# Performance work log

Measured on AMD Instinct MI355X. Metric: run time of the kernel, lower is better.

The kernel has to match this reference:

```python
import jax, jax.numpy as jnp
import numpy as np
from jax import lax

H = 1024
E = 8
TOP_K = 2


def setup_inputs() -> dict:
    key = jax.random.key(0)
    kx, k1, k2 = jax.random.split(key, 3)
    x = jax.random.normal(kx, (8, 2048, H), dtype=jnp.float32)
    # router MLP params, init normal(0, 0.02), zero bias (matches _init_weights)
    w1 = jax.random.normal(k1, (H, 2 * H), dtype=jnp.float32) * 0.02
    b1 = jnp.zeros((2 * H,), dtype=jnp.float32)
    w2 = jax.random.normal(k2, (2 * H, E), dtype=jnp.float32) * 0.02
    b2 = jnp.zeros((E,), dtype=jnp.float32)
    return {"x": x, "w1": w1, "b1": b1, "w2": w2, "b2": b2}


def reference(x, w1, b1, w2, b2):
    # gating MLP: Linear -> GELU (exact, torch default) -> Linear
    h = jax.nn.gelu(jnp.einsum('bsh,hf->bsf', x, w1) + b1, approximate=False)
    expert_weights = jnp.einsum('bsf,fe->bse', h, w2) + b2  # [B,S,E]

    top_k_weights, top_k_indices = lax.top_k(expert_weights, TOP_K)  # [B,S,K]
    top_k_weights = jax.nn.softmax(top_k_weights, axis=-1)

    # scatter renormalized weights into dense [B,S,E] mask (indices distinct -> one-hot sum)
    onehot = jax.nn.one_hot(top_k_indices, E, dtype=expert_weights.dtype)  # [B,S,K,E]
    masks = jnp.einsum('bsk,bske->bse', top_k_weights, onehot)

    expert_usage = masks.sum(axis=(0, 1))
    expert_usage = expert_usage / expert_usage.sum()
    target_usage = jnp.full_like(expert_usage, 1.0 / E)
    load_balancing_loss = jnp.mean((expert_usage - target_usage) ** 2)

    sparsity_loss = jnp.mean(jnp.sum(masks > 0, axis=-1).astype(jnp.float32)) / TOP_K
    total_loss = load_balancing_loss + 0.1 * sparsity_loss

    return expert_weights, masks, total_loss, expert_usage
```

## Files before the change

### kernel.cpp

```cpp
#include <hip/hip_runtime.h>
#include <math.h>

#define HDIM 1024
#define FDIM 2048
#define NEXP 8
#define MTOK 16384
#define NSLC 32
#define LDSB 24576
#define LDS_BYTES (3 * 49152)

typedef __attribute__((ext_vector_type(8))) short bf16x8;
typedef __attribute__((ext_vector_type(4))) float f32x4;

__device__ inline unsigned short f2bf_rne(float f) {
    unsigned int u = __float_as_uint(f);
    u = (u + 0x7FFFu + ((u >> 16) & 1u)) >> 16;
    return (unsigned short)u;
}
__device__ inline float bf2f(unsigned short h) {
    unsigned int u = ((unsigned int)h) << 16;
    return __uint_as_float(u);
}

__global__ __launch_bounds__(256) void cvt_x(const float* __restrict__ x,
                                             unsigned short* __restrict__ af)
{
    __shared__ unsigned short hs[16384];
    __shared__ unsigned short ls[16384];
    const int mt = blockIdx.x;
    const float* src = x + (size_t)mt * 16384;
    const int m = threadIdx.x & 15;
    const int kseg = threadIdx.x >> 4;

    #pragma unroll
    for (int c = 0; c < 8; c++) {
        int k = c * 128 + kseg * 8;
        float v[8];
        *(float4*)(v)     = *(const float4*)(src + m * 1024 + k);
        *(float4*)(v + 4) = *(const float4*)(src + m * 1024 + k + 4);
        union { unsigned short u[8]; uint4 q; } oh, ol;
        #pragma unroll
        for (int j = 0; j < 8; j++) {
            unsigned short h = f2bf_rne(v[j]);
            oh.u[j] = h;
            ol.u[j] = f2bf_rne(v[j] - bf2f(h));
        }
        int kb = k >> 5, q = (k >> 3) & 3;
        int o = kb * 512 + m * 32 + q * 8;
        *(uint4*)(hs + o) = oh.q;
        *(uint4*)(ls + o) = ol.q;
    }
    __syncthreads();
    unsigned short* dst = af + (size_t)mt * 32768;
    #pragma unroll
    for (int c = 0; c < 16; c++) {
        int f = c * 2048 + threadIdx.x * 8;
        int kb = f >> 10, half = (f >> 9) & 1, idx = f & 511;
        int q = idx >> 7, mm = (idx >> 3) & 15;
        const unsigned short* s = (half ? ls : hs) + kb * 512 + mm * 32 + q * 8;
        *(uint4*)(dst + f) = *(const uint4*)s;
    }
}

__global__ __launch_bounds__(256) void cvt_w1f(const float* __restrict__ w1,
                                               unsigned short* __restrict__ wf)
{
    __shared__ float t[32][33];
    int n0 = blockIdx.x * 32;
    int k0 = blockIdx.y * 32;
    int lx = threadIdx.x & 31, ly = threadIdx.x >> 5;
    #pragma unroll
    for (int r = 0; r < 32; r += 8)
        t[ly + r][lx] = w1[(size_t)(k0 + ly + r) * FDIM + n0 + lx];
    __syncthreads();
    #pragma unroll
    for (int r = 0; r < 32; r += 8) {
        float v = t[lx][ly + r];
        unsigned short h = f2bf_rne(v);
        unsigned short l = f2bf_rne(v - bf2f(h));
        int n = n0 + ly + r, k = k0 + lx;
        size_t base = (size_t)((n >> 4) * 32 + (k >> 5)) * 1024;
        int lj = (((k >> 3) & 3) * 16 + (n & 15)) * 8 + (k & 7);
        wf[base + lj] = h;
        wf[base + 512 + lj] = l;
    }
}

#define GLDX4(gp, lofs) __builtin_amdgcn_global_load_lds( \
    (const __attribute__((address_space(1))) unsigned int*)(uintptr_t)(gp), \
    (__attribute__((address_space(3))) unsigned int*)(unsigned int)(uintptr_t)(smem + (lofs)), \
    16, 0, 0)

__global__ __launch_bounds__(512, 2) void gemm1_mfma(
    const unsigned short* __restrict__ af, const unsigned short* __restrict__ wf,
    const float* __restrict__ b1, const float* __restrict__ w2,
    float* __restrict__ part)
{
    extern __shared__ unsigned short smem[];
    const int tid  = threadIdx.x;
    const int lane = tid & 63;
    const int l15  = lane & 15;
    const int q    = lane >> 4;
    const int wave = tid >> 6;
    const int wm   = wave >> 1;
    const int wn   = wave & 1;

    const int id  = blockIdx.x;
    const int xcd = id & 7, seq = id >> 3;
    const int bn  = seq & 15;
    const int bm  = xcd * 8 + (seq >> 4);
    const int m0  = bm * 256, n0g = bn * 128;

    const unsigned short* gb[6];
    int lo[6];
    #pragma unroll
    for (int s = 0; s < 6; s++) {
        int c = wave * 6 + s;
        int f = c >> 1, half = c & 1;
        const unsigned short* base = (f < 16)
            ? af + (size_t)(bm * 16 + f) * 32768
            : wf + (size_t)(bn * 8 + (f - 16)) * 32768;
        gb[s] = base + half * 512 + lane * 8;
        lo[s] = f * 1024 + half * 512;
    }

    f32x4 acc[4][4];
    #pragma unroll
    for (int i = 0; i < 4; i++)
        #pragma unroll
        for (int j = 0; j < 4; j++) acc[i][j] = (f32x4){0.f, 0.f, 0.f, 0.f};

    #pragma unroll
    for (int s = 0; s < 6; s++) GLDX4(gb[s], lo[s]);
    #pragma unroll
    for (int s = 0; s < 6; s++) GLDX4(gb[s] + 1024, LDSB + lo[s]);
    asm volatile("s_waitcnt vmcnt(6)\n\ts_barrier" ::: "memory");

    int bo = 0;
    #pragma unroll 1
    for (int t = 0; t < 32; t++) {
        int bi = bo + 2 * LDSB; if (bi >= 3 * LDSB) bi -= 3 * LDSB;
        if (t + 2 < 32) {
            #pragma unroll
            for (int s = 0; s < 6; s++)
                GLDX4(gb[s] + (size_t)(t + 2) * 1024, bi + lo[s]);
        }
        const unsigned short* sb = smem + bo;
        bf16x8 Bh[4], Bl[4];
        #pragma unroll
        for (int j = 0; j < 4; j++) {
            Bh[j] = *(const bf16x8*)(sb + (16 + wn * 4 + j) * 1024 + lane * 8);
            Bl[j] = *(const bf16x8*)(sb + (16 + wn * 4 + j) * 1024 + 512 + lane * 8);
        }
        __builtin_amdgcn_s_setprio(1);
        #pragma unroll
        for (int ih = 0; ih < 2; ih++) {
            bf16x8 Ah[2], Al[2];
            #pragma unroll
            for (int i = 0; i < 2; i++) {
                int mt = wm * 4 + ih * 2 + i;
                Ah[i] = *(const bf16x8*)(sb + mt * 1024 + lane * 8);
                Al[i] = *(const bf16x8*)(sb + mt * 1024 + 512 + lane * 8);
            }
            #pragma unroll
            for (int i = 0; i < 2; i++)
                #pragma unroll
                for (int j = 0; j < 4; j++) {
                    f32x4 a = acc[ih * 2 + i][j];
                    a = __builtin_amdgcn_mfma_f32_16x16x32_bf16(Ah[i], Bh[j], a, 0, 0, 0);
                    a = __builtin_amdgcn_mfma_f32_16x16x32_bf16(Ah[i], Bl[j], a, 0, 0, 0);
                    a = __builtin_amdgcn_mfma_f32_16x16x32_bf16(Al[i], Bh[j], a, 0, 0, 0);
                    acc[ih * 2 + i][j] = a;
                }
        }
        __builtin_amdgcn_s_setprio(0);
        bo += LDSB; if (bo >= 3 * LDSB) bo -= 3 * LDSB;
        if (t < 30)       asm volatile("s_waitcnt vmcnt(6)\n\ts_barrier" ::: "memory");
        else if (t == 30) asm volatile("s_waitcnt vmcnt(0)\n\ts_barrier" ::: "memory");
    }

    #pragma unroll
    for (int j = 0; j < 4; j++) {
        int n = n0g + wn * 64 + j * 16 + l15;
        float bb = b1[n];
        #pragma unroll
        for (int i = 0; i < 4; i++)
            #pragma unroll
            for (int r = 0; r < 4; r++) {
                float v = acc[i][j][r] + bb;
                acc[i][j][r] = 0.5f * v * (1.0f + erff(v * 0.70710678118654752f));
            }
    }

    float w2r[4][8];
    #pragma unroll
    for (int j = 0; j < 4; j++) {
        const float4* p = (const float4*)(w2 + (size_t)(n0g + wn * 64 + j * 16 + l15) * NEXP);
        float4 u = p[0], v = p[1];
        w2r[j][0] = u.x; w2r[j][1] = u.y; w2r[j][2] = u.z; w2r[j][3] = u.w;
        w2r[j][4] = v.x; w2r[j][5] = v.y; w2r[j][6] = v.z; w2r[j][7] = v.w;
    }

    const int sl = bn * 2 + wn;
    #pragma unroll
    for (int e = 0; e < NEXP; e++) {
        float p[4][4];
        #pragma unroll
        for (int i = 0; i < 4; i++)
            #pragma unroll
            for (int r = 0; r < 4; r++) {
                float s = 0.f;
                #pragma unroll
                for (int j = 0; j < 4; j++) s += acc[i][j][r] * w2r[j][e];
                p[i][r] = s;
            }
        #pragma unroll
        for (int off = 1; off < 16; off <<= 1)
            #pragma unroll
            for (int i = 0; i < 4; i++)
                #pragma unroll
                for (int r = 0; r < 4; r++)
                    p[i][r] += __shfl_xor(p[i][r], off);
        if (l15 == 0) {
            #pragma unroll
            for (int i = 0; i < 4; i++)
                #pragma unroll
                for (int r = 0; r < 4; r++) {
                    int m = m0 + wm * 64 + i * 16 + q * 4 + r;
                    part[(size_t)sl * (MTOK * NEXP) + (size_t)m * NEXP + e] = p[i][r];
                }
        }
    }
}

__global__ __launch_bounds__(256) void router_topk(
    const float* __restrict__ part, const float* __restrict__ b2,
    float* __restrict__ out, float* __restrict__ gu, int* __restrict__ gc)
{
    const int t = blockIdx.x * 256 + threadIdx.x;

    float logit[8];
    #pragma unroll
    for (int e = 0; e < 8; e++) logit[e] = b2[e];
    #pragma unroll
    for (int j = 0; j < NSLC; j++) {
        const float4* p4 = (const float4*)(part + (size_t)j * (MTOK * NEXP) + (size_t)t * NEXP);
        float4 u = p4[0], v = p4[1];
        logit[0] += u.x; logit[1] += u.y; logit[2] += u.z; logit[3] += u.w;
        logit[4] += v.x; logit[5] += v.y; logit[6] += v.z; logit[7] += v.w;
    }

    int i1 = 0; float v1 = logit[0];
    #pragma unroll
    for (int e = 1; e < 8; e++) { if (logit[e] > v1) { v1 = logit[e]; i1 = e; } }
    int i2 = -1; float v2 = -INFINITY;
    #pragma unroll
    for (int e = 0; e < 8; e++) {
        if (e != i1 && logit[e] > v2) { v2 = logit[e]; i2 = e; }
    }
    float ex = expf(v2 - v1);
    float inv = 1.0f / (1.0f + ex);
    float wa = inv, wb = ex * inv;

    float4* o = (float4*)(out + (size_t)t * NEXP);
    o[0] = make_float4(logit[0], logit[1], logit[2], logit[3]);
    o[1] = make_float4(logit[4], logit[5], logit[6], logit[7]);

    float mk[8];
    #pragma unroll
    for (int e = 0; e < 8; e++) mk[e] = 0.0f;
    mk[i1] = wa; mk[i2] = wb;
    float4* om = (float4*)(out + (size_t)(MTOK * NEXP) + (size_t)t * NEXP);
    om[0] = make_float4(mk[0], mk[1], mk[2], mk[3]);
    om[1] = make_float4(mk[4], mk[5], mk[6], mk[7]);

    __shared__ float us[8];
    __shared__ int cs;
    if (threadIdx.x < 8) us[threadIdx.x] = 0.0f;
    if (threadIdx.x == 0) cs = 0;
    __syncthreads();
    atomicAdd(&us[i1], wa);
    atomicAdd(&us[i2], wb);
    int cnt = (wa > 0.0f ? 1 : 0) + (wb > 0.0f ? 1 : 0);
    atomicAdd(&cs, cnt);
    __syncthreads();
    if (threadIdx.x < 8) atomicAdd(&gu[threadIdx.x], us[threadIdx.x]);
    if (threadIdx.x == 0) atomicAdd(gc, cs);
}

__global__ void router_final(const float* __restrict__ gu, const int* __restrict__ gc,
                             float* __restrict__ out)
{
    if (blockIdx.x == 0 && threadIdx.x == 0) {
        float u[8]; float tot = 0.0f;
        for (int e = 0; e < 8; e++) { u[e] = gu[e]; tot += u[e]; }
        float lb = 0.0f;
        for (int e = 0; e < 8; e++) {
            float un = u[e] / tot;
            out[2 * MTOK * NEXP + 1 + e] = un;
            float d = un - 0.125f;
            lb += d * d;
        }
        lb *= (1.0f / 8.0f);
        float sp = ((float)(*gc) / (float)MTOK) * 0.5f;
        out[2 * MTOK * NEXP] = lb + 0.1f * sp;
    }
}

extern "C" void kernel_launch(void* const* d_in, const int* in_sizes, int n_in,
                              void* d_out, int out_size, void* d_ws, size_t ws_size,
                              hipStream_t stream) {
    const float* x  = (const float*)d_in[0];
    const float* w1 = (const float*)d_in[1];
    const float* b1 = (const float*)d_in[2];
    const float* w2 = (const float*)d_in[3];
    const float* b2 = (const float*)d_in[4];
    float* out = (float*)d_out;

    unsigned short* af = (unsigned short*)d_ws;
    unsigned short* wf = af + (size_t)1024 * 32768;
    float* part = (float*)(wf + (size_t)128 * 32 * 1024);
    float* gu = part + (size_t)NSLC * MTOK * NEXP;
    int* gc = (int*)(gu + 8);

    static bool attr_done = false;
    if (!attr_done) {
        hipFuncSetAttribute((const void*)gemm1_mfma,
                            hipFuncAttributeMaxDynamicSharedMemorySize, LDS_BYTES);
        attr_done = true;
    }

    hipMemsetAsync(gu, 0, 64, stream);

    cvt_x<<<1024, 256, 0, stream>>>(x, af);
    cvt_w1f<<<dim3(FDIM / 32, HDIM / 32), 256, 0, stream>>>(w1, wf);
    gemm1_mfma<<<1024, 512, LDS_BYTES, stream>>>(af, wf, b1, w2, part);
    router_topk<<<MTOK / 256, 256, 0, stream>>>(part, b2, out, gu, gc);
    router_final<<<1, 64, 0, stream>>>(gu, gc, out);
}
```

Measured before the change: 360.5 us.

## Interleave LDS reads, global prefetch and MFMA in four barrier-separated phases

```diff
diff --git a/kernel.cpp b/kernel.cpp
--- a/kernel.cpp
+++ b/kernel.cpp
@@ -140,40 +140,46 @@
     #pragma unroll 1
     for (int t = 0; t < 32; t++) {
         int bi = bo + 2 * LDSB; if (bi >= 3 * LDSB) bi -= 3 * LDSB;
-        if (t + 2 < 32) {
-            #pragma unroll
-            for (int s = 0; s < 6; s++)
-                GLDX4(gb[s] + (size_t)(t + 2) * 1024, bi + lo[s]);
+        const unsigned short* sb = smem + bo;
+        const size_t goff = (size_t)(t + 2) * 1024;
+        bf16x8 Ah[4], Al[4];
+        #pragma unroll
+        for (int j = 0; j < 4; j++) {
+            if (j == 0) {
+                #pragma unroll
+                for (int i = 0; i < 4; i++) {
+                    const unsigned short* ap = sb + (wm * 4 + i) * 1024 + lane * 8;
+                    Ah[i] = *(const bf16x8*)(ap);
+                    Al[i] = *(const bf16x8*)(ap + 512);
+                }
+            }
+            const unsigned short* bp = sb + (16 + wn * 4 + j) * 1024 + lane * 8;
+            bf16x8 Bh = *(const bf16x8*)(bp);
+            bf16x8 Bl = *(const bf16x8*)(bp + 512);
+            if (t + 2 < 32) {
+                if (j < 2) {
+                    GLDX4(gb[2 * j]     + goff, bi + lo[2 * j]);
+                    GLDX4(gb[2 * j + 1] + goff, bi + lo[2 * j + 1]);
+                } else {
+                    GLDX4(gb[j + 2] + goff, bi + lo[j + 2]);
+                }
+            }
+            __builtin_amdgcn_s_barrier();
+            asm volatile("s_waitcnt lgkmcnt(0)" ::: "memory");
+            __builtin_amdgcn_sched_barrier(0);
+            __builtin_amdgcn_s_setprio(1);
+            #pragma unroll
+            for (int i = 0; i < 4; i++) {
+                f32x4 a = acc[i][j];
+                a = __builtin_amdgcn_mfma_f32_16x16x32_bf16(Ah[i], Bh, a, 0, 0, 0);
+                a = __builtin_amdgcn_mfma_f32_16x16x32_bf16(Ah[i], Bl, a, 0, 0, 0);
+                a = __builtin_amdgcn_mfma_f32_16x16x32_bf16(Al[i], Bh, a, 0, 0, 0);
+                acc[i][j] = a;
+            }
+            __builtin_amdgcn_s_setprio(0);
+            __builtin_amdgcn_sched_barrier(0);
+            if (j < 3) __builtin_amdgcn_s_barrier();
         }
-        const unsigned short* sb = smem + bo;
-        bf16x8 Bh[4], Bl[4];
-        #pragma unroll
-        for (int j = 0; j < 4; j++) {
-            Bh[j] = *(const bf16x8*)(sb + (16 + wn * 4 + j) * 1024 + lane * 8);
-            Bl[j] = *(const bf16x8*)(sb + (16 + wn * 4 + j) * 1024 + 512 + lane * 8);
-        }
-        __builtin_amdgcn_s_setprio(1);
-        #pragma unroll
-        for (int ih = 0; ih < 2; ih++) {
-            bf16x8 Ah[2], Al[2];
-            #pragma unroll
-            for (int i = 0; i < 2; i++) {
-                int mt = wm * 4 + ih * 2 + i;
-                Ah[i] = *(const bf16x8*)(sb + mt * 1024 + lane * 8);
-                Al[i] = *(const bf16x8*)(sb + mt * 1024 + 512 + lane * 8);
-            }
-            #pragma unroll
-            for (int i = 0; i < 2; i++)
-                #pragma unroll
-                for (int j = 0; j < 4; j++) {
-                    f32x4 a = acc[ih * 2 + i][j];
-                    a = __builtin_amdgcn_mfma_f32_16x16x32_bf16(Ah[i], Bh[j], a, 0, 0, 0);
-                    a = __builtin_amdgcn_mfma_f32_16x16x32_bf16(Ah[i], Bl[j], a, 0, 0, 0);
-                    a = __builtin_amdgcn_mfma_f32_16x16x32_bf16(Al[i], Bh[j], a, 0, 0, 0);
-                    acc[ih * 2 + i][j] = a;
-                }
-        }
-        __builtin_amdgcn_s_setprio(0);
         bo += LDSB; if (bo >= 3 * LDSB) bo -= 3 * LDSB;
         if (t < 30)       asm volatile("s_waitcnt vmcnt(6)\n\ts_barrier" ::: "memory");
         else if (t == 30) asm volatile("s_waitcnt vmcnt(0)\n\ts_barrier" ::: "memory");
```

New measurement: 368.8 us. +2.3%, slower.

## Double-buffer LDS fragment reads in registers to overlap with MFMA

Applied to the files above, without the earlier changes.

```diff
diff --git a/kernel.cpp b/kernel.cpp
--- a/kernel.cpp
+++ b/kernel.cpp
@@ -91,6 +91,36 @@
     (__attribute__((address_space(3))) unsigned int*)(unsigned int)(uintptr_t)(smem + (lofs)), \
     16, 0, 0)
 
+#define READ_KB(sb, AH, AL, BH, BL) \
+    do { \
+        _Pragma("unroll") \
+        for (int i_ = 0; i_ < 4; i_++) { \
+            const unsigned short* ap_ = (sb) + (wm * 4 + i_) * 1024 + lane * 8; \
+            AH[i_] = *(const bf16x8*)(ap_); \
+            AL[i_] = *(const bf16x8*)(ap_ + 512); \
+        } \
+        _Pragma("unroll") \
+        for (int j_ = 0; j_ < 4; j_++) { \
+            const unsigned short* bp_ = (sb) + (16 + wn * 4 + j_) * 1024 + lane * 8; \
+            BH[j_] = *(const bf16x8*)(bp_); \
+            BL[j_] = *(const bf16x8*)(bp_ + 512); \
+        } \
+    } while (0)
+
+#define MFMA_KB(AH, AL, BH, BL) \
+    do { \
+        _Pragma("unroll") \
+        for (int i_ = 0; i_ < 4; i_++) \
+            _Pragma("unroll") \
+            for (int j_ = 0; j_ < 4; j_++) { \
+                f32x4 a_ = acc[i_][j_]; \
+                a_ = __builtin_amdgcn_mfma_f32_16x16x32_bf16(AH[i_], BH[j_], a_, 0, 0, 0); \
+                a_ = __builtin_amdgcn_mfma_f32_16x16x32_bf16(AH[i_], BL[j_], a_, 0, 0, 0); \
+                a_ = __builtin_amdgcn_mfma_f32_16x16x32_bf16(AL[i_], BH[j_], a_, 0, 0, 0); \
+                acc[i_][j_] = a_; \
+            } \
+    } while (0)
+
 __global__ __launch_bounds__(512, 2) void gemm1_mfma(
     const unsigned short* __restrict__ af, const unsigned short* __restrict__ wf,
     const float* __restrict__ b1, const float* __restrict__ w2,
@@ -136,47 +166,45 @@
     for (int s = 0; s < 6; s++) GLDX4(gb[s] + 1024, LDSB + lo[s]);
     asm volatile("s_waitcnt vmcnt(6)\n\ts_barrier" ::: "memory");
 
+    bf16x8 Ah0[4], Al0[4], Bh0[4], Bl0[4];
+    bf16x8 Ah1[4], Al1[4], Bh1[4], Bl1[4];
+    READ_KB(smem, Ah0, Al0, Bh0, Bl0);
+
     int bo = 0;
     #pragma unroll 1
-    for (int t = 0; t < 32; t++) {
-        int bi = bo + 2 * LDSB; if (bi >= 3 * LDSB) bi -= 3 * LDSB;
-        if (t + 2 < 32) {
-            #pragma unroll
-            for (int s = 0; s < 6; s++)
-                GLDX4(gb[s] + (size_t)(t + 2) * 1024, bi + lo[s]);
-        }
-        const unsigned short* sb = smem + bo;
-        bf16x8 Bh[4], Bl[4];
-        #pragma unroll
-        for (int j = 0; j < 4; j++) {
-            Bh[j] = *(const bf16x8*)(sb + (16 + wn * 4 + j) * 1024 + lane * 8);
-            Bl[j] = *(const bf16x8*)(sb + (16 + wn * 4 + j) * 1024 + 512 + lane * 8);
-        }
-        __builtin_amdgcn_s_setprio(1);
-        #pragma unroll
-        for (int ih = 0; ih < 2; ih++) {
-            bf16x8 Ah[2], Al[2];
-            #pragma unroll
-            for (int i = 0; i < 2; i++) {
-                int mt = wm * 4 + ih * 2 + i;
-                Ah[i] = *(const bf16x8*)(sb + mt * 1024 + lane * 8);
-                Al[i] = *(const bf16x8*)(sb + mt * 1024 + 512 + lane * 8);
-            }
-            #pragma unroll
-            for (int i = 0; i < 2; i++)
-                #pragma unroll
-                for (int j = 0; j < 4; j++) {
-                    f32x4 a = acc[ih * 2 + i][j];
-                    a = __builtin_amdgcn_mfma_f32_16x16x32_bf16(Ah[i], Bh[j], a, 0, 0, 0);
-                    a = __builtin_amdgcn_mfma_f32_16x16x32_bf16(Ah[i], Bl[j], a, 0, 0, 0);
-                    a = __builtin_amdgcn_mfma_f32_16x16x32_bf16(Al[i], Bh[j], a, 0, 0, 0);
-                    acc[ih * 2 + i][j] = a;
-                }
-        }
-        __builtin_amdgcn_s_setprio(0);
-        bo += LDSB; if (bo >= 3 * LDSB) bo -= 3 * LDSB;
-        if (t < 30)       asm volatile("s_waitcnt vmcnt(6)\n\ts_barrier" ::: "memory");
-        else if (t == 30) asm volatile("s_waitcnt vmcnt(0)\n\ts_barrier" ::: "memory");
+    for (int t = 0; t < 32; t += 2) {
+        {
+            int bi = bo + 2 * LDSB; if (bi >= 3 * LDSB) bi -= 3 * LDSB;
+            if (t + 2 < 32) {
+                const size_t go = (size_t)(t + 2) * 1024;
+                #pragma unroll
+                for (int s = 0; s < 6; s++) GLDX4(gb[s] + go, bi + lo[s]);
+                asm volatile("s_waitcnt vmcnt(6)\n\ts_barrier" ::: "memory");
+            } else {
+                asm volatile("s_waitcnt vmcnt(0)\n\ts_barrier" ::: "memory");
+            }
+            int bnx = bo + LDSB; if (bnx >= 3 * LDSB) bnx -= 3 * LDSB;
+            READ_KB(smem + bnx, Ah1, Al1, Bh1, Bl1);
+            MFMA_KB(Ah0, Al0, Bh0, Bl0);
+            bo = bnx;
+        }
+        {
+            int bi = bo + 2 * LDSB; if (bi >= 3 * LDSB) bi -= 3 * LDSB;
+            if (t + 3 < 32) {
+                const size_t go = (size_t)(t + 3) * 1024;
+                #pragma unroll
+                for (int s = 0; s < 6; s++) GLDX4(gb[s] + go, bi + lo[s]);
+            }
+            if (t + 2 < 32) {
+                asm volatile("s_waitcnt vmcnt(6)\n\ts_barrier" ::: "memory");
+                int bnx = bo + LDSB; if (bnx >= 3 * LDSB) bnx -= 3 * LDSB;
+                READ_KB(smem + bnx, Ah0, Al0, Bh0, Bl0);
+                MFMA_KB(Ah1, Al1, Bh1, Bl1);
+                bo = bnx;
+            } else {
+                MFMA_KB(Ah1, Al1, Bh1, Bl1);
+            }
+        }
     }
 
     #pragma unroll
```

New measurement: 445.4 us. +23.6%, slower.

## Split main GEMM loop into three barrier-fenced phases per split-bf16 product

Applied to the files above, without the earlier changes.

```diff
diff --git a/kernel.cpp b/kernel.cpp
--- a/kernel.cpp
+++ b/kernel.cpp
@@ -140,40 +140,65 @@
     #pragma unroll 1
     for (int t = 0; t < 32; t++) {
         int bi = bo + 2 * LDSB; if (bi >= 3 * LDSB) bi -= 3 * LDSB;
+        const unsigned short* sb = smem + bo;
+        bf16x8 Ah[4], Bh[4], Al[4], Bl[4];
+
+        #pragma unroll
+        for (int i = 0; i < 4; i++)
+            Ah[i] = *(const bf16x8*)(sb + (wm * 4 + i) * 1024 + lane * 8);
+        #pragma unroll
+        for (int j = 0; j < 4; j++)
+            Bh[j] = *(const bf16x8*)(sb + (16 + wn * 4 + j) * 1024 + lane * 8);
         if (t + 2 < 32) {
-            #pragma unroll
-            for (int s = 0; s < 6; s++)
-                GLDX4(gb[s] + (size_t)(t + 2) * 1024, bi + lo[s]);
+            const size_t goff = (size_t)(t + 2) * 1024;
+            #pragma unroll
+            for (int s = 0; s < 6; s++) GLDX4(gb[s] + goff, bi + lo[s]);
         }
-        const unsigned short* sb = smem + bo;
-        bf16x8 Bh[4], Bl[4];
-        #pragma unroll
-        for (int j = 0; j < 4; j++) {
-            Bh[j] = *(const bf16x8*)(sb + (16 + wn * 4 + j) * 1024 + lane * 8);
+        __builtin_amdgcn_s_barrier();
+        asm volatile("s_waitcnt lgkmcnt(0)" ::: "memory");
+        __builtin_amdgcn_sched_barrier(0);
+        __builtin_amdgcn_s_setprio(1);
+        #pragma unroll
+        for (int i = 0; i < 4; i++)
+            #pragma unroll
+            for (int j = 0; j < 4; j++)
+                acc[i][j] = __builtin_amdgcn_mfma_f32_16x16x32_bf16(
+                    Ah[i], Bh[j], acc[i][j], 0, 0, 0);
+        __builtin_amdgcn_s_setprio(0);
+        __builtin_amdgcn_sched_barrier(0);
+
+        #pragma unroll
+        for (int j = 0; j < 4; j++)
             Bl[j] = *(const bf16x8*)(sb + (16 + wn * 4 + j) * 1024 + 512 + lane * 8);
-        }
+        __builtin_amdgcn_s_barrier();
+        asm volatile("s_waitcnt lgkmcnt(0)" ::: "memory");
+        __builtin_amdgcn_sched_barrier(0);
         __builtin_amdgcn_s_setprio(1);
         #pragma unroll
-        for (int ih = 0; ih < 2; ih++) {
-            bf16x8 Ah[2], Al[2];
-            #pragma unroll
-            for (int i = 0; i < 2; i++) {
-                int mt = wm * 4 + ih * 2 + i;
-                Ah[i] = *(const bf16x8*)(sb + mt * 1024 + lane * 8);
-                Al[i] = *(const bf16x8*)(sb + mt * 1024 + 512 + lane * 8);
-            }
-            #pragma unroll
-            for (int i = 0; i < 2; i++)
-                #pragma unroll
-                for (int j = 0; j < 4; j++) {
-                    f32x4 a = acc[ih * 2 + i][j];
-                    a = __builtin_amdgcn_mfma_f32_16x16x32_bf16(Ah[i], Bh[j], a, 0, 0, 0);
-                    a = __builtin_amdgcn_mfma_f32_16x16x32_bf16(Ah[i], Bl[j], a, 0, 0, 0);
-                    a = __builtin_amdgcn_mfma_f32_16x16x32_bf16(Al[i], Bh[j], a, 0, 0, 0);
-                    acc[ih * 2 + i][j] = a;
-                }
-        }
+        for (int i = 0; i < 4; i++)
+            #pragma unroll
+            for (int j = 0; j < 4; j++)
+                acc[i][j] = __builtin_amdgcn_mfma_f32_16x16x32_bf16(
+                    Ah[i], Bl[j], acc[i][j], 0, 0, 0);
         __builtin_amdgcn_s_setprio(0);
+        __builtin_amdgcn_sched_barrier(0);
+
+        #pragma unroll
+        for (int i = 0; i < 4; i++)
+            Al[i] = *(const bf16x8*)(sb + (wm * 4 + i) * 1024 + 512 + lane * 8);
+        __builtin_amdgcn_s_barrier();
+        asm volatile("s_waitcnt lgkmcnt(0)" ::: "memory");
+        __builtin_amdgcn_sched_barrier(0);
+        __builtin_amdgcn_s_setprio(1);
+        #pragma unroll
+        for (int i = 0; i < 4; i++)
+            #pragma unroll
+            for (int j = 0; j < 4; j++)
+                acc[i][j] = __builtin_amdgcn_mfma_f32_16x16x32_bf16(
+                    Al[i], Bh[j], acc[i][j], 0, 0, 0);
+        __builtin_amdgcn_s_setprio(0);
+        __builtin_amdgcn_sched_barrier(0);
+
         bo += LDSB; if (bo >= 3 * LDSB) bo -= 3 * LDSB;
         if (t < 30)       asm volatile("s_waitcnt vmcnt(6)\n\ts_barrier" ::: "memory");
         else if (t == 30) asm volatile("s_waitcnt vmcnt(0)\n\ts_barrier" ::: "memory");
```

New measurement: 361.7 us. No clear change (+0.3%).
